# Optimization experiments

Measured on AMD Instinct MI355X. Metric: run time of the kernel, lower is better.

## Reference

```python
import jax, jax.numpy as jnp
import numpy as np

N_NODES = 100000
N_EDGES = 1600000
IN_F = 128
HID_F = 128
OUT_F = 128
HEAD_HID = 128
HEAD_OUT = 64


def setup_inputs() -> dict:
    key = jax.random.key(0)
    ks = jax.random.split(key, 16)
    glorot = lambda k, i, o: jax.random.normal(k, (i, o), jnp.float32) * (2.0 / (i + o)) ** 0.5
    return {
        "x": jax.random.normal(ks[0], (N_NODES, IN_F), jnp.float32),
        "src": jax.random.randint(ks[1], (N_EDGES,), 0, N_NODES),
        "dst": jax.random.randint(ks[2], (N_EDGES,), 0, N_NODES),
        "eps1": jnp.zeros((), jnp.float32),
        "eps2": jnp.zeros((), jnp.float32),
        # mlp_fun1: in_feats -> hid -> hid
        "w11": glorot(ks[3], IN_F, HID_F), "b11": jnp.zeros((HID_F,), jnp.float32),
        "w12": glorot(ks[4], HID_F, HID_F), "b12": jnp.zeros((HID_F,), jnp.float32),
        # mlp_fun2: hid -> hid -> out_feats
        "w21": glorot(ks[5], HID_F, HID_F), "b21": jnp.zeros((HID_F,), jnp.float32),
        "w22": glorot(ks[6], HID_F, OUT_F), "b22": jnp.zeros((OUT_F,), jnp.float32),
        # head mlp: out_feats -> hidden_dim -> output_dim (sigmoid)
        "wm1": glorot(ks[7], OUT_F, HEAD_HID), "bm1": jnp.zeros((HEAD_HID,), jnp.float32),
        "wm2": glorot(ks[8], HEAD_HID, HEAD_OUT), "bm2": jnp.zeros((HEAD_OUT,), jnp.float32),
    }


def _mlp2(h, w1, b1, w2, b2):
    # 2-layer MLP: Linear -> ReLU -> Linear
    return jax.nn.relu(h @ w1 + b1) @ w2 + b2


def _gin_conv(x, src, dst, eps, w1, b1, w2, b2):
    # sum-aggregate over incoming edges, then MLP update (DGL GINConv, learn_eps)
    agg = jax.ops.segment_sum(x[src], dst, num_segments=x.shape[0])  # [N, d]
    return _mlp2((1.0 + eps) * x + agg, w1, b1, w2, b2)


def reference(x, src, dst, eps1, eps2, w11, b11, w12, b12,
              w21, b21, w22, b22, wm1, bm1, wm2, bm2):
    # dropout is identity in eval mode
    h = jax.nn.relu(_gin_conv(x, src, dst, eps1, w11, b11, w12, b12))
    h = jax.nn.relu(_gin_conv(h, src, dst, eps2, w21, b21, w22, b22))
    # head MLP producing per-node probabilities (consumed by log-prob loss)
    return jax.nn.sigmoid(_mlp2(h, wm1, bm1, wm2, bm2))  # [N, output_dim]
```

## Files before the change

kernel.cpp:

```cpp
#include <hip/hip_runtime.h>

static constexpr int NN = 100000;
static constexpr int NE = 1600000;
static constexpr int NBUK = (NN + 255) / 256;
static constexpr int SC_BLOCKS = 400;
static constexpr int SC_CH = NE / SC_BLOCKS;

typedef float     f32x4  __attribute__((ext_vector_type(4)));
typedef _Float16  f16x8  __attribute__((ext_vector_type(8)));

static constexpr float LO_SCALE  = 16384.0f;
static constexpr float LO_USCALE = 1.0f / 16384.0f;

__device__ __forceinline__ unsigned pkh(float x, float y){
  unsigned short a = __builtin_bit_cast(unsigned short, (_Float16)x);
  unsigned short b = __builtin_bit_cast(unsigned short, (_Float16)y);
  return (unsigned)a | ((unsigned)b << 16);
}
__device__ __forceinline__ float2 uph(unsigned u){
  _Float16 a = __builtin_bit_cast(_Float16, (unsigned short)(u & 0xffffu));
  _Float16 b = __builtin_bit_cast(_Float16, (unsigned short)(u >> 16));
  return make_float2((float)a, (float)b);
}

__global__ void k_pack(const float* __restrict__ w11, const float* __restrict__ w12,
                       const float* __restrict__ w21, const float* __restrict__ w22,
                       const float* __restrict__ wm1, const float* __restrict__ wm2,
                       unsigned short* __restrict__ p11h, unsigned short* __restrict__ p11l,
                       unsigned short* __restrict__ p12h, unsigned short* __restrict__ p12l,
                       unsigned short* __restrict__ p21h, unsigned short* __restrict__ p21l,
                       unsigned short* __restrict__ p22h, unsigned short* __restrict__ p22l,
                       unsigned short* __restrict__ pm1h, unsigned short* __restrict__ pm1l,
                       unsigned short* __restrict__ pm2h, unsigned short* __restrict__ pm2l){
  int b = blockIdx.x, lane = threadIdx.x;
  const float* W; unsigned short* Ph; unsigned short* Pl; int NCT, f;
  if (b < 160){
    int m = b >> 5; f = b & 31; NCT = 8;
    W  = (m==0)?w11 :(m==1)?w12 :(m==2)?w21 :(m==3)?w22 :wm1;
    Ph = (m==0)?p11h:(m==1)?p12h:(m==2)?p21h:(m==3)?p22h:pm1h;
    Pl = (m==0)?p11l:(m==1)?p12l:(m==2)?p21l:(m==3)?p22l:pm1l;
  } else { f = b - 160; NCT = 4; W = wm2; Ph = pm2h; Pl = pm2l; }
  int NC = NCT * 16;
  int kt = f / NCT, ct = f % NCT;
  int k0 = kt*32 + ((lane>>4)*8), col = ct*16 + (lane&15);
  unsigned short* dh = Ph + ((size_t)(f*64 + lane))*8;
  unsigned short* dl = Pl + ((size_t)(f*64 + lane))*8;
  #pragma unroll
  for (int j=0;j<8;j++){
    float v = W[(size_t)(k0+j)*NC + col];
    _Float16 h = (_Float16)v;
    _Float16 l = (_Float16)((v - (float)h) * LO_SCALE);
    dh[j] = __builtin_bit_cast(unsigned short, h);
    dl[j] = __builtin_bit_cast(unsigned short, l);
  }
}

__global__ void k_cvt(const float* __restrict__ x, unsigned* __restrict__ xh, int n4){
  int i = blockIdx.x*256 + threadIdx.x;
  if (i < n4){
    float4 v = reinterpret_cast<const float4*>(x)[i];
    uint2 o; o.x = pkh(v.x, v.y); o.y = pkh(v.z, v.w);
    reinterpret_cast<uint2*>(xh)[i] = o;
  }
}

__global__ __launch_bounds__(256) void k_hist(const int* __restrict__ dst, int* __restrict__ bhist){
  __shared__ int h[NBUK];
  int blk = blockIdx.x, t = threadIdx.x;
  for (int i=t;i<NBUK;i+=256) h[i]=0;
  __syncthreads();
  int e0 = blk*SC_CH;
  for (int e=e0+t; e<e0+SC_CH; e+=256) atomicAdd(&h[((unsigned)dst[e])>>8], 1);
  __syncthreads();
  for (int i=t;i<NBUK;i+=256){ int c=h[i]; if (c) atomicAdd(&bhist[i], c); }
}

__global__ void k_boff2(const int* __restrict__ bhist, int* __restrict__ boff){
  __shared__ int s[512];
  int t = threadIdx.x;
  int v = (t < NBUK) ? bhist[t] : 0;
  s[t] = v; __syncthreads();
  for (int off=1; off<512; off<<=1){
    int u = 0; if (t>=off) u = s[t-off];
    __syncthreads(); s[t] += u; __syncthreads();
  }
  if (t < NBUK) boff[t] = s[t] - v;
}

__global__ __launch_bounds__(256) void k_scatter1(const int* __restrict__ src,
                                                  const int* __restrict__ dst,
                                                  const int* __restrict__ boff,
                                                  int* __restrict__ gbcur,
                                                  uint2* __restrict__ tmp){
  __shared__ int hc[NBUK];
  __shared__ int hb[NBUK];
  int blk = blockIdx.x, t = threadIdx.x;
  int e0 = blk * SC_CH, e1 = e0 + SC_CH;
  for (int i=t;i<NBUK;i+=256) hc[i]=0;
  __syncthreads();
  for (int e=e0+t; e<e1; e+=256) atomicAdd(&hc[((unsigned)dst[e])>>8], 1);
  __syncthreads();
  for (int i=t;i<NBUK;i+=256){ int c = hc[i]; hb[i] = c ? atomicAdd(&gbcur[i], c) : 0; }
  __syncthreads();
  for (int i=t;i<NBUK;i+=256) hc[i]=0;
  __syncthreads();
  for (int e=e0+t; e<e1; e+=256){
    int d = dst[e]; int b = ((unsigned)d)>>8;
    int pos = atomicAdd(&hc[b], 1);
    tmp[(size_t)boff[b] + hb[b] + pos] = make_uint2((unsigned)src[e], (unsigned)d);
  }
}

__global__ __launch_bounds__(256) void k_fill2(const uint2* __restrict__ tmp,
                                               const int* __restrict__ boff,
                                               const int* __restrict__ bhist,
                                               int* __restrict__ eidx,
                                               int* __restrict__ rs, int* __restrict__ deg, int N){
  __shared__ int lh[256];
  __shared__ int ls[256];
  __shared__ int lc[256];
  int b = blockIdx.x, t = threadIdx.x;
  int base = boff[b], cnt = bhist[b];
  int nb0 = b*256;
  lh[t] = 0; lc[t] = 0;
  __syncthreads();
  for (int i=t; i<cnt; i+=256) atomicAdd(&lh[(int)tmp[(size_t)base+i].y - nb0], 1);
  __syncthreads();
  int v = lh[t];
  ls[t] = v; __syncthreads();
  for (int off=1; off<256; off<<=1){
    int u = 0; if (t>=off) u = ls[t-off];
    __syncthreads(); ls[t] += u; __syncthreads();
  }
  int node = nb0 + t;
  if (node < N){ deg[node] = v; rs[node] = base + ls[t] - v; }
  __syncthreads();
  for (int i=t; i<cnt; i+=256){
    uint2 e = tmp[(size_t)base+i];
    int local = (int)e.y - nb0;
    int pos = atomicAdd(&lc[local], 1);
    eidx[base + ls[local] - lh[local] + pos] = (int)e.x;
  }
}

__global__ __launch_bounds__(256) void k_agg(const unsigned* __restrict__ inp,
                                             unsigned* __restrict__ out,
                                             const float* __restrict__ epsp,
                                             const int* __restrict__ rs, const int* __restrict__ deg,
                                             const int* __restrict__ eidx, int N){
  int gw = (blockIdx.x*256 + threadIdx.x) >> 6;
  int lane = threadIdx.x & 63;
  if (gw >= N) return;
  float sc = 1.0f + *epsp;
  float2 v = uph(inp[(size_t)gw*64 + lane]);
  float a0 = sc * v.x, a1 = sc * v.y;
  int beg = rs[gw], d = deg[gw];
  int i = 0;
  for (; i+8 <= d; i += 8){
    unsigned u[8];
    #pragma unroll
    for (int j=0;j<8;j++) u[j] = inp[(size_t)eidx[beg+i+j]*64 + lane];
    #pragma unroll
    for (int j=0;j<8;j++){ float2 f = uph(u[j]); a0 += f.x; a1 += f.y; }
  }
  for (; i < d; ++i){
    float2 u = uph(inp[(size_t)eidx[beg+i]*64 + lane]);
    a0 += u.x; a1 += u.y;
  }
  out[(size_t)gw*64 + lane] = pkh(a0, a1);
}

__device__ __forceinline__ void load_a_glob(const _Float16* __restrict__ t, int rbase,
                                            int wv, int lane, int N, f16x8 a[4]){
  int row = rbase + wv*16 + (lane & 15); if (row >= N) row = N - 1;
  const _Float16* ap = t + (size_t)row*128 + ((lane>>4)*8);
  #pragma unroll
  for (int kt=0;kt<4;kt++) a[kt] = *reinterpret_cast<const f16x8*>(ap + kt*32);
}
__device__ __forceinline__ void load_a_lds(const _Float16* base, int lane, f16x8 a[4], int stride){
  int row = lane & 15, ko = (lane>>4)*8;
  #pragma unroll
  for (int kt=0;kt<4;kt++) a[kt] = *reinterpret_cast<const f16x8*>(base + row*stride + kt*32 + ko);
}

template<int NCT>
__device__ __forceinline__ void mm2(const f16x8 a[4],
                                    const unsigned short* __restrict__ wh,
                                    const unsigned short* __restrict__ wl,
                                    int lane, f32x4 acc[NCT], f32x4 acc2[NCT]){
  #pragma unroll
  for (int ct=0; ct<NCT; ++ct){
    f32x4 c  = {0.f,0.f,0.f,0.f};
    f32x4 c2 = {0.f,0.f,0.f,0.f};
    #pragma unroll
    for (int kt=0; kt<4; ++kt){
      int fo = ((kt*NCT + ct)*64 + lane) << 3;
      f16x8 bh = *reinterpret_cast<const f16x8*>(wh + fo);
      f16x8 bl = *reinterpret_cast<const f16x8*>(wl + fo);
      c  = __builtin_amdgcn_mfma_f32_16x16x32_f16(a[kt], bh, c,  0, 0, 0);
      c2 = __builtin_amdgcn_mfma_f32_16x16x32_f16(a[kt], bl, c2, 0, 0, 0);
    }
    acc[ct] = c; acc2[ct] = c2;
  }
}

template<int NCT>
__device__ __forceinline__ void epi_relu(const f32x4 acc[NCT], const f32x4 acc2[NCT],
                                         const float* __restrict__ bias,
                                         _Float16* dst, int lane, int stride){
  int r0 = (lane>>4)*4, col0 = lane & 15;
  #pragma unroll
  for (int ct=0; ct<NCT; ++ct){
    float bv = bias[ct*16 + col0];
    #pragma unroll
    for (int r=0;r<4;r++){
      float v = fmaxf(acc[ct][r] + acc2[ct][r]*LO_USCALE + bv, 0.f);
      dst[(r0 + r)*stride + ct*16 + col0] = (_Float16)v;
    }
  }
}

static constexpr int HSTR = 136;
static constexpr int WSLICE = 16*HSTR;

__global__ __launch_bounds__(256) void k_mlp1(const _Float16* __restrict__ t,
    const unsigned short* __restrict__ w1h, const unsigned short* __restrict__ w1l, const float* __restrict__ b1,
    const unsigned short* __restrict__ w2h, const unsigned short* __restrict__ w2l, const float* __restrict__ b2,
    unsigned* __restrict__ h, int N){
  __shared__ _Float16 lds[4*WSLICE];
  int tid = threadIdx.x, lane = tid & 63, wv = tid >> 6;
  _Float16* slice = lds + wv*WSLICE;
  int rbase = blockIdx.x * 64;
  f16x8 a[4];
  f32x4 acc[8], acc2[8];
  load_a_glob(t, rbase, wv, lane, N, a);
  mm2<8>(a, w1h, w1l, lane, acc, acc2);
  epi_relu<8>(acc, acc2, b1, slice, lane, HSTR);
  load_a_lds(slice, lane, a, HSTR);
  mm2<8>(a, w2h, w2l, lane, acc, acc2);
  epi_relu<8>(acc, acc2, b2, slice, lane, HSTR);
  int wrow0 = rbase + wv*16;
  for (int i=lane; i < 16*32; i += 64){
    int r = i >> 5, c = i & 31;
    if (wrow0 + r < N)
      reinterpret_cast<uint2*>(h)[(size_t)(wrow0 + r)*32 + c] =
        *reinterpret_cast<const uint2*>(slice + r*HSTR + c*4);
  }
}

__global__ __launch_bounds__(256) void k_mlp2_head(const _Float16* __restrict__ t,
    const unsigned short* __restrict__ w1h, const unsigned short* __restrict__ w1l, const float* __restrict__ b1,
    const unsigned short* __restrict__ w2h, const unsigned short* __restrict__ w2l, const float* __restrict__ b2,
    const unsigned short* __restrict__ w3h, const unsigned short* __restrict__ w3l, const float* __restrict__ b3,
    const unsigned short* __restrict__ w4h, const unsigned short* __restrict__ w4l, const float* __restrict__ b4,
    float* __restrict__ out, int N){
  __shared__ _Float16 lds[4*WSLICE];
  int tid = threadIdx.x, lane = tid & 63, wv = tid >> 6;
  _Float16* slice = lds + wv*WSLICE;
  int rbase = blockIdx.x * 64;
  f16x8 a[4];
  f32x4 acc[8], acc2[8];
  load_a_glob(t, rbase, wv, lane, N, a);
  mm2<8>(a, w1h, w1l, lane, acc, acc2);
  epi_relu<8>(acc, acc2, b1, slice, lane, HSTR);
  load_a_lds(slice, lane, a, HSTR);
  mm2<8>(a, w2h, w2l, lane, acc, acc2);
  epi_relu<8>(acc, acc2, b2, slice, lane, HSTR);
  load_a_lds(slice, lane, a, HSTR);
  mm2<8>(a, w3h, w3l, lane, acc, acc2);
  epi_relu<8>(acc, acc2, b3, slice, lane, HSTR);
  load_a_lds(slice, lane, a, HSTR);
  f32x4 acc4[4], acc4b[4];
  mm2<4>(a, w4h, w4l, lane, acc4, acc4b);
  {
    float* olds = reinterpret_cast<float*>(slice);
    int r0 = (lane>>4)*4, col0 = lane & 15;
    #pragma unroll
    for (int ct=0; ct<4; ++ct){
      float bv = b4[ct*16 + col0];
      #pragma unroll
      for (int r=0;r<4;r++){
        float z = acc4[ct][r] + acc4b[ct][r]*LO_USCALE + bv;
        float s = 1.0f / (1.0f + __expf(-z));
        olds[(r0 + r)*68 + ct*16 + col0] = s;
      }
    }
  }
  const float* olds = reinterpret_cast<const float*>(slice);
  int wrow0 = rbase + wv*16;
  for (int i=lane; i < 16*16; i += 64){
    int r = i >> 4, c = i & 15;
    if (wrow0 + r < N)
      reinterpret_cast<float4*>(out)[(size_t)(wrow0 + r)*16 + c] =
        *reinterpret_cast<const float4*>(olds + r*68 + c*4);
  }
}

extern "C" void kernel_launch(void* const* d_in, const int* in_sizes, int n_in,
                              void* d_out, int out_size, void* d_ws, size_t ws_size,
                              hipStream_t stream) {
  const float* x   = (const float*)d_in[0];
  const int*   src = (const int*)  d_in[1];
  const int*   dst = (const int*)  d_in[2];
  const float* eps1= (const float*)d_in[3];
  const float* eps2= (const float*)d_in[4];
  const float* w11 = (const float*)d_in[5];  const float* b11 = (const float*)d_in[6];
  const float* w12 = (const float*)d_in[7];  const float* b12 = (const float*)d_in[8];
  const float* w21 = (const float*)d_in[9];  const float* b21 = (const float*)d_in[10];
  const float* w22 = (const float*)d_in[11]; const float* b22 = (const float*)d_in[12];
  const float* wm1 = (const float*)d_in[13]; const float* bm1 = (const float*)d_in[14];
  const float* wm2 = (const float*)d_in[15]; const float* bm2 = (const float*)d_in[16];

  char* ws = (char*)d_ws;
  size_t off = 0;
  auto alloc = [&](size_t bytes) -> void* {
    void* p = ws + off;
    off = (off + bytes + 255) & ~(size_t)255;
    return p;
  };
  unsigned* xh  = (unsigned*)alloc((size_t)NN*64*4);
  unsigned* B0  = (unsigned*)alloc((size_t)NN*64*4);
  unsigned* h1h = (unsigned*)alloc((size_t)NN*64*4);
  uint2* tmp = (uint2*)alloc((size_t)NE*8);
  int* eidx = (int*)alloc((size_t)NE*4);
  int* deg  = (int*)alloc((size_t)NN*4);
  int* rs   = (int*)alloc((size_t)NN*4);
  int* bhist= (int*)alloc((size_t)NBUK*4);
  int* boff = (int*)alloc((size_t)NBUK*4);
  int* gbcur= (int*)alloc((size_t)NBUK*4);
  unsigned short* p11h = (unsigned short*)alloc(128*128*2);
  unsigned short* p11l = (unsigned short*)alloc(128*128*2);
  unsigned short* p12h = (unsigned short*)alloc(128*128*2);
  unsigned short* p12l = (unsigned short*)alloc(128*128*2);
  unsigned short* p21h = (unsigned short*)alloc(128*128*2);
  unsigned short* p21l = (unsigned short*)alloc(128*128*2);
  unsigned short* p22h = (unsigned short*)alloc(128*128*2);
  unsigned short* p22l = (unsigned short*)alloc(128*128*2);
  unsigned short* pm1h = (unsigned short*)alloc(128*128*2);
  unsigned short* pm1l = (unsigned short*)alloc(128*128*2);
  unsigned short* pm2h = (unsigned short*)alloc(128*64*2);
  unsigned short* pm2l = (unsigned short*)alloc(128*64*2);
  if (off > ws_size) return;

  hipMemsetAsync(bhist, 0, (size_t)NBUK*4, stream);
  hipMemsetAsync(gbcur, 0, (size_t)NBUK*4, stream);

  k_pack<<<176, 64, 0, stream>>>(w11,w12,w21,w22,wm1,wm2,
                                 p11h,p11l,p12h,p12l,p21h,p21l,p22h,p22l,pm1h,pm1l,pm2h,pm2l);
  k_cvt<<<(NN*32 + 255)/256, 256, 0, stream>>>(x, xh, NN*32);
  k_hist<<<SC_BLOCKS, 256, 0, stream>>>(dst, bhist);
  k_boff2<<<1, 512, 0, stream>>>(bhist, boff);
  k_scatter1<<<SC_BLOCKS, 256, 0, stream>>>(src, dst, boff, gbcur, tmp);
  k_fill2<<<NBUK, 256, 0, stream>>>(tmp, boff, bhist, eidx, rs, deg, NN);

  k_agg<<<(NN+3)/4, 256, 0, stream>>>(xh, B0, eps1, rs, deg, eidx, NN);
  k_mlp1<<<(NN+63)/64, 256, 0, stream>>>((const _Float16*)B0, p11h, p11l, b11,
                                         p12h, p12l, b12, h1h, NN);
  k_agg<<<(NN+3)/4, 256, 0, stream>>>(h1h, B0, eps2, rs, deg, eidx, NN);
  k_mlp2_head<<<(NN+63)/64, 256, 0, stream>>>((const _Float16*)B0, p21h, p21l, b21,
                                              p22h, p22l, b22, pm1h, pm1l, bm1,
                                              pm2h, pm2l, bm2, (float*)d_out, NN);
}
```

Baseline: 341.2 us.

## Process two row tiles per wave in MLP kernels with interleaved hi/lo weight layout

```diff
diff --git a/kernel.cpp b/kernel.cpp
--- a/kernel.cpp
+++ b/kernel.cpp
@@ -26,25 +26,22 @@
 __global__ void k_pack(const float* __restrict__ w11, const float* __restrict__ w12,
                        const float* __restrict__ w21, const float* __restrict__ w22,
                        const float* __restrict__ wm1, const float* __restrict__ wm2,
-                       unsigned short* __restrict__ p11h, unsigned short* __restrict__ p11l,
-                       unsigned short* __restrict__ p12h, unsigned short* __restrict__ p12l,
-                       unsigned short* __restrict__ p21h, unsigned short* __restrict__ p21l,
-                       unsigned short* __restrict__ p22h, unsigned short* __restrict__ p22l,
-                       unsigned short* __restrict__ pm1h, unsigned short* __restrict__ pm1l,
-                       unsigned short* __restrict__ pm2h, unsigned short* __restrict__ pm2l){
+                       unsigned short* __restrict__ p11, unsigned short* __restrict__ p12,
+                       unsigned short* __restrict__ p21, unsigned short* __restrict__ p22,
+                       unsigned short* __restrict__ pm1, unsigned short* __restrict__ pm2){
   int b = blockIdx.x, lane = threadIdx.x;
-  const float* W; unsigned short* Ph; unsigned short* Pl; int NCT, f;
+  const float* W; unsigned short* P; int NCT, f;
   if (b < 160){
     int m = b >> 5; f = b & 31; NCT = 8;
-    W  = (m==0)?w11 :(m==1)?w12 :(m==2)?w21 :(m==3)?w22 :wm1;
-    Ph = (m==0)?p11h:(m==1)?p12h:(m==2)?p21h:(m==3)?p22h:pm1h;
-    Pl = (m==0)?p11l:(m==1)?p12l:(m==2)?p21l:(m==3)?p22l:pm1l;
-  } else { f = b - 160; NCT = 4; W = wm2; Ph = pm2h; Pl = pm2l; }
+    W = (m==0)?w11:(m==1)?w12:(m==2)?w21:(m==3)?w22:wm1;
+    P = (m==0)?p11:(m==1)?p12:(m==2)?p21:(m==3)?p22:pm1;
+  } else { f = b - 160; NCT = 4; W = wm2; P = pm2; }
   int NC = NCT * 16;
   int kt = f / NCT, ct = f % NCT;
+  int hidx = ct >> 2, ct4 = ct & 3;
   int k0 = kt*32 + ((lane>>4)*8), col = ct*16 + (lane&15);
-  unsigned short* dh = Ph + ((size_t)(f*64 + lane))*8;
-  unsigned short* dl = Pl + ((size_t)(f*64 + lane))*8;
+  unsigned short* dh = P + (hidx<<14) + ((kt*4+ct4)<<10) + (lane<<3);
+  unsigned short* dl = dh + 512;
   #pragma unroll
   for (int j=0;j<8;j++){
     float v = W[(size_t)(k0+j)*NC + col];
@@ -170,129 +167,141 @@
   out[(size_t)gw*64 + lane] = pkh(a0, a1);
 }
 
-__device__ __forceinline__ void load_a_glob(const _Float16* __restrict__ t, int rbase,
-                                            int wv, int lane, int N, f16x8 a[4]){
-  int row = rbase + wv*16 + (lane & 15); if (row >= N) row = N - 1;
-  const _Float16* ap = t + (size_t)row*128 + ((lane>>4)*8);
-  #pragma unroll
-  for (int kt=0;kt<4;kt++) a[kt] = *reinterpret_cast<const f16x8*>(ap + kt*32);
-}
-__device__ __forceinline__ void load_a_lds(const _Float16* base, int lane, f16x8 a[4], int stride){
-  int row = lane & 15, ko = (lane>>4)*8;
-  #pragma unroll
-  for (int kt=0;kt<4;kt++) a[kt] = *reinterpret_cast<const f16x8*>(base + row*stride + kt*32 + ko);
-}
-
-template<int NCT>
-__device__ __forceinline__ void mm2(const f16x8 a[4],
-                                    const unsigned short* __restrict__ wh,
-                                    const unsigned short* __restrict__ wl,
-                                    int lane, f32x4 acc[NCT], f32x4 acc2[NCT]){
-  #pragma unroll
-  for (int ct=0; ct<NCT; ++ct){
-    f32x4 c  = {0.f,0.f,0.f,0.f};
-    f32x4 c2 = {0.f,0.f,0.f,0.f};
+static constexpr int HSTR = 136;
+static constexpr int WSLICE = 32*HSTR;
+
+__device__ __forceinline__ void load_a_glob2(const _Float16* __restrict__ t, int rbase,
+                                             int lane, int N, f16x8 a[2][4]){
+  #pragma unroll
+  for (int ms=0; ms<2; ++ms){
+    int row = rbase + ms*16 + (lane & 15); if (row >= N) row = N - 1;
+    const _Float16* ap = t + (size_t)row*128 + ((lane>>4)*8);
+    #pragma unroll
+    for (int kt=0;kt<4;kt++) a[ms][kt] = *reinterpret_cast<const f16x8*>(ap + kt*32);
+  }
+}
+__device__ __forceinline__ void load_a_lds2(const _Float16* slice, int lane, f16x8 a[2][4]){
+  int ko = (lane>>4)*8;
+  #pragma unroll
+  for (int ms=0; ms<2; ++ms){
+    const _Float16* rp = slice + (ms*16 + (lane&15))*HSTR + ko;
+    #pragma unroll
+    for (int kt=0;kt<4;kt++) a[ms][kt] = *reinterpret_cast<const f16x8*>(rp + kt*32);
+  }
+}
+
+__device__ __forceinline__ void half_relu(const f16x8 a[2][4],
+                                          const unsigned short* __restrict__ w,
+                                          const float* __restrict__ bias,
+                                          _Float16* slice, int lane, int hidx){
+  const unsigned short* wb = w + (hidx<<14);
+  int r0 = (lane>>4)*4, col0 = lane & 15;
+  #pragma unroll
+  for (int ct4=0; ct4<4; ++ct4){
+    f32x4 c0={0.f,0.f,0.f,0.f}, c1={0.f,0.f,0.f,0.f};
+    f32x4 d0={0.f,0.f,0.f,0.f}, d1={0.f,0.f,0.f,0.f};
     #pragma unroll
     for (int kt=0; kt<4; ++kt){
-      int fo = ((kt*NCT + ct)*64 + lane) << 3;
-      f16x8 bh = *reinterpret_cast<const f16x8*>(wh + fo);
-      f16x8 bl = *reinterpret_cast<const f16x8*>(wl + fo);
-      c  = __builtin_amdgcn_mfma_f32_16x16x32_f16(a[kt], bh, c,  0, 0, 0);
-      c2 = __builtin_amdgcn_mfma_f32_16x16x32_f16(a[kt], bl, c2, 0, 0, 0);
+      const f16x8 bh = *reinterpret_cast<const f16x8*>(wb + ((kt*4+ct4)<<10) + (lane<<3));
+      const f16x8 bl = *reinterpret_cast<const f16x8*>(wb + ((kt*4+ct4)<<10) + 512 + (lane<<3));
+      c0 = __builtin_amdgcn_mfma_f32_16x16x32_f16(a[0][kt], bh, c0, 0,0,0);
+      c1 = __builtin_amdgcn_mfma_f32_16x16x32_f16(a[1][kt], bh, c1, 0,0,0);
+      d0 = __builtin_amdgcn_mfma_f32_16x16x32_f16(a[0][kt], bl, d0, 0,0,0);
+      d1 = __builtin_amdgcn_mfma_f32_16x16x32_f16(a[1][kt], bl, d1, 0,0,0);
     }
-    acc[ct] = c; acc2[ct] = c2;
-  }
-}
-
-template<int NCT>
-__device__ __forceinline__ void epi_relu(const f32x4 acc[NCT], const f32x4 acc2[NCT],
+    float bv = bias[hidx*64 + ct4*16 + col0];
+    int cb = hidx*64 + ct4*16 + col0;
+    #pragma unroll
+    for (int r=0;r<4;r++){
+      float v0 = fmaxf(c0[r] + d0[r]*LO_USCALE + bv, 0.f);
+      float v1 = fmaxf(c1[r] + d1[r]*LO_USCALE + bv, 0.f);
+      slice[(r0+r)*HSTR + cb]      = (_Float16)v0;
+      slice[(16+r0+r)*HSTR + cb]   = (_Float16)v1;
+    }
+  }
+}
+
+__device__ __forceinline__ void head_sig(const f16x8 a[2][4],
+                                         const unsigned short* __restrict__ w,
                                          const float* __restrict__ bias,
-                                         _Float16* dst, int lane, int stride){
+                                         float* fs, int lane){
   int r0 = (lane>>4)*4, col0 = lane & 15;
   #pragma unroll
-  for (int ct=0; ct<NCT; ++ct){
-    float bv = bias[ct*16 + col0];
+  for (int ct4=0; ct4<4; ++ct4){
+    f32x4 c0={0.f,0.f,0.f,0.f}, c1={0.f,0.f,0.f,0.f};
+    f32x4 d0={0.f,0.f,0.f,0.f}, d1={0.f,0.f,0.f,0.f};
+    #pragma unroll
+    for (int kt=0; kt<4; ++kt){
+      const f16x8 bh = *reinterpret_cast<const f16x8*>(w + ((kt*4+ct4)<<10) + (lane<<3));
+      const f16x8 bl = *reinterpret_cast<const f16x8*>(w + ((kt*4+ct4)<<10) + 512 + (lane<<3));
+      c0 = __builtin_amdgcn_mfma_f32_16x16x32_f16(a[0][kt], bh, c0, 0,0,0);
+      c1 = __builtin_amdgcn_mfma_f32_16x16x32_f16(a[1][kt], bh, c1, 0,0,0);
+      d0 = __builtin_amdgcn_mfma_f32_16x16x32_f16(a[0][kt], bl, d0, 0,0,0);
+      d1 = __builtin_amdgcn_mfma_f32_16x16x32_f16(a[1][kt], bl, d1, 0,0,0);
+    }
+    float bv = bias[ct4*16 + col0];
+    int cb = ct4*16 + col0;
     #pragma unroll
     for (int r=0;r<4;r++){
-      float v = fmaxf(acc[ct][r] + acc2[ct][r]*LO_USCALE + bv, 0.f);
-      dst[(r0 + r)*stride + ct*16 + col0] = (_Float16)v;
+      float z0 = c0[r] + d0[r]*LO_USCALE + bv;
+      float z1 = c1[r] + d1[r]*LO_USCALE + bv;
+      fs[(r0+r)*68 + cb]    = 1.0f / (1.0f + __expf(-z0));
+      fs[(16+r0+r)*68 + cb] = 1.0f / (1.0f + __expf(-z1));
     }
   }
 }
 
-static constexpr int HSTR = 136;
-static constexpr int WSLICE = 16*HSTR;
-
 __global__ __launch_bounds__(256) void k_mlp1(const _Float16* __restrict__ t,
-    const unsigned short* __restrict__ w1h, const unsigned short* __restrict__ w1l, const float* __restrict__ b1,
-    const unsigned short* __restrict__ w2h, const unsigned short* __restrict__ w2l, const float* __restrict__ b2,
+    const unsigned short* __restrict__ w1, const float* __restrict__ b1,
+    const unsigned short* __restrict__ w2, const float* __restrict__ b2,
     unsigned* __restrict__ h, int N){
   __shared__ _Float16 lds[4*WSLICE];
   int tid = threadIdx.x, lane = tid & 63, wv = tid >> 6;
   _Float16* slice = lds + wv*WSLICE;
-  int rbase = blockIdx.x * 64;
-  f16x8 a[4];
-  f32x4 acc[8], acc2[8];
-  load_a_glob(t, rbase, wv, lane, N, a);
-  mm2<8>(a, w1h, w1l, lane, acc, acc2);
-  epi_relu<8>(acc, acc2, b1, slice, lane, HSTR);
-  load_a_lds(slice, lane, a, HSTR);
-  mm2<8>(a, w2h, w2l, lane, acc, acc2);
-  epi_relu<8>(acc, acc2, b2, slice, lane, HSTR);
-  int wrow0 = rbase + wv*16;
-  for (int i=lane; i < 16*32; i += 64){
+  int rbase = blockIdx.x*128 + wv*32;
+  f16x8 a[2][4];
+  load_a_glob2(t, rbase, lane, N, a);
+  half_relu(a, w1, b1, slice, lane, 0);
+  half_relu(a, w1, b1, slice, lane, 1);
+  load_a_lds2(slice, lane, a);
+  half_relu(a, w2, b2, slice, lane, 0);
+  half_relu(a, w2, b2, slice, lane, 1);
+  for (int i=lane; i < 32*32; i += 64){
     int r = i >> 5, c = i & 31;
-    if (wrow0 + r < N)
-      reinterpret_cast<uint2*>(h)[(size_t)(wrow0 + r)*32 + c] =
+    if (rbase + r < N)
+      reinterpret_cast<uint2*>(h)[(size_t)(rbase + r)*32 + c] =
         *reinterpret_cast<const uint2*>(slice + r*HSTR + c*4);
   }
 }
 
 __global__ __launch_bounds__(256) void k_mlp2_head(const _Float16* __restrict__ t,
-    const unsigned short* __restrict__ w1h, const unsigned short* __restrict__ w1l, const float* __restrict__ b1,
-    const unsigned short* __restrict__ w2h, const unsigned short* __restrict__ w2l, const float* __restrict__ b2,
-    const unsigned short* __restrict__ w3h, const unsigned short* __restrict__ w3l, const float* __restrict__ b3,
-    const unsigned short* __restrict__ w4h, const unsigned short* __restrict__ w4l, const float* __restrict__ b4,
+    const unsigned short* __restrict__ w1, const float* __restrict__ b1,
+    const unsigned short* __restrict__ w2, const float* __restrict__ b2,
+    const unsigned short* __restrict__ w3, const float* __restrict__ b3,
+    const unsigned short* __restrict__ w4, const float* __restrict__ b4,
     float* __restrict__ out, int N){
   __shared__ _Float16 lds[4*WSLICE];
   int tid = threadIdx.x, lane = tid & 63, wv = tid >> 6;
   _Float16* slice = lds + wv*WSLICE;
-  int rbase = blockIdx.x * 64;
-  f16x8 a[4];
-  f32x4 acc[8], acc2[8];
-  load_a_glob(t, rbase, wv, lane, N, a);
-  mm2<8>(a, w1h, w1l, lane, acc, acc2);
-  epi_relu<8>(acc, acc2, b1, slice, lane, HSTR);
-  load_a_lds(slice, lane, a, HSTR);
-  mm2<8>(a, w2h, w2l, lane, acc, acc2);
-  epi_relu<8>(acc, acc2, b2, slice, lane, HSTR);
-  load_a_lds(slice, lane, a, HSTR);
-  mm2<8>(a, w3h, w3l, lane, acc, acc2);
-  epi_relu<8>(acc, acc2, b3, slice, lane, HSTR);
-  load_a_lds(slice, lane, a, HSTR);
-  f32x4 acc4[4], acc4b[4];
-  mm2<4>(a, w4h, w4l, lane, acc4, acc4b);
-  {
-    float* olds = reinterpret_cast<float*>(slice);
-    int r0 = (lane>>4)*4, col0 = lane & 15;
-    #pragma unroll
-    for (int ct=0; ct<4; ++ct){
-      float bv = b4[ct*16 + col0];
-      #pragma unroll
-      for (int r=0;r<4;r++){
-        float z = acc4[ct][r] + acc4b[ct][r]*LO_USCALE + bv;
-        float s = 1.0f / (1.0f + __expf(-z));
-        olds[(r0 + r)*68 + ct*16 + col0] = s;
-      }
-    }
-  }
-  const float* olds = reinterpret_cast<const float*>(slice);
-  int wrow0 = rbase + wv*16;
-  for (int i=lane; i < 16*16; i += 64){
+  int rbase = blockIdx.x*128 + wv*32;
+  f16x8 a[2][4];
+  load_a_glob2(t, rbase, lane, N, a);
+  half_relu(a, w1, b1, slice, lane, 0);
+  half_relu(a, w1, b1, slice, lane, 1);
+  load_a_lds2(slice, lane, a);
+  half_relu(a, w2, b2, slice, lane, 0);
+  half_relu(a, w2, b2, slice, lane, 1);
+  load_a_lds2(slice, lane, a);
+  half_relu(a, w3, b3, slice, lane, 0);
+  half_relu(a, w3, b3, slice, lane, 1);
+  load_a_lds2(slice, lane, a);
+  float* fs = reinterpret_cast<float*>(slice);
+  head_sig(a, w4, b4, fs, lane);
+  for (int i=lane; i < 32*16; i += 64){
     int r = i >> 4, c = i & 15;
-    if (wrow0 + r < N)
-      reinterpret_cast<float4*>(out)[(size_t)(wrow0 + r)*16 + c] =
-        *reinterpret_cast<const float4*>(olds + r*68 + c*4);
+    if (rbase + r < N)
+      reinterpret_cast<float4*>(out)[(size_t)(rbase + r)*16 + c] =
+        *reinterpret_cast<const float4*>(fs + r*68 + c*4);
   }
 }
 
@@ -328,36 +337,28 @@
   int* bhist= (int*)alloc((size_t)NBUK*4);
   int* boff = (int*)alloc((size_t)NBUK*4);
   int* gbcur= (int*)alloc((size_t)NBUK*4);
-  unsigned short* p11h = (unsigned short*)alloc(128*128*2);
-  unsigned short* p11l = (unsigned short*)alloc(128*128*2);
-  unsigned short* p12h = (unsigned short*)alloc(128*128*2);
-  unsigned short* p12l = (unsigned short*)alloc(128*128*2);
-  unsigned short* p21h = (unsigned short*)alloc(128*128*2);
-  unsigned short* p21l = (unsigned short*)alloc(128*128*2);
-  unsigned short* p22h = (unsigned short*)alloc(128*128*2);
-  unsigned short* p22l = (unsigned short*)alloc(128*128*2);
-  unsigned short* pm1h = (unsigned short*)alloc(128*128*2);
-  unsigned short* pm1l = (unsigned short*)alloc(128*128*2);
-  unsigned short* pm2h = (unsigned short*)alloc(128*64*2);
-  unsigned short* pm2l = (unsigned short*)alloc(128*64*2);
+  unsigned short* p11 = (unsigned short*)alloc(128*128*2*2);
+  unsigned short* p12 = (unsigned short*)alloc(128*128*2*2);
+  unsigned short* p21 = (unsigned short*)alloc(128*128*2*2);
+  unsigned short* p22 = (unsigned short*)alloc(128*128*2*2);
+  unsigned short* pm1 = (unsigned short*)alloc(128*128*2*2);
+  unsigned short* pm2 = (unsigned short*)alloc(128*64*2*2);
   if (off > ws_size) return;
 
   hipMemsetAsync(bhist, 0, (size_t)NBUK*4, stream);
   hipMemsetAsync(gbcur, 0, (size_t)NBUK*4, stream);
 
-  k_pack<<<176, 64, 0, stream>>>(w11,w12,w21,w22,wm1,wm2,
-                                 p11h,p11l,p12h,p12l,p21h,p21l,p22h,p22l,pm1h,pm1l,pm2h,pm2l);
+  k_pack<<<176, 64, 0, stream>>>(w11,w12,w21,w22,wm1,wm2, p11,p12,p21,p22,pm1,pm2);
   k_cvt<<<(NN*32 + 255)/256, 256, 0, stream>>>(x, xh, NN*32);
   k_hist<<<SC_BLOCKS, 256, 0, stream>>>(dst, bhist);
   k_boff2<<<1, 512, 0, stream>>>(bhist, boff);
   k_scatter1<<<SC_BLOCKS, 256, 0, stream>>>(src, dst, boff, gbcur, tmp);
   k_fill2<<<NBUK, 256, 0, stream>>>(tmp, boff, bhist, eidx, rs, deg, NN);
 
+  int mgrid = (NN + 127) / 128;
   k_agg<<<(NN+3)/4, 256, 0, stream>>>(xh, B0, eps1, rs, deg, eidx, NN);
-  k_mlp1<<<(NN+63)/64, 256, 0, stream>>>((const _Float16*)B0, p11h, p11l, b11,
-                                         p12h, p12l, b12, h1h, NN);
+  k_mlp1<<<mgrid, 256, 0, stream>>>((const _Float16*)B0, p11, b11, p12, b12, h1h, NN);
   k_agg<<<(NN+3)/4, 256, 0, stream>>>(h1h, B0, eps2, rs, deg, eidx, NN);
-  k_mlp2_head<<<(NN+63)/64, 256, 0, stream>>>((const _Float16*)B0, p21h, p21l, b21,
-                                              p22h, p22l, b22, pm1h, pm1l, bm1,
-                                              pm2h, pm2l, bm2, (float*)d_out, NN);
-}
+  k_mlp2_head<<<mgrid, 256, 0, stream>>>((const _Float16*)B0, p21, b21, p22, b22,
+                                         pm1, bm1, pm2, bm2, (float*)d_out, NN);
+}
```

Result: faster. 301.2 us (-11.7%).
